# Performance work log

Hardware: AMD Instinct MI355X
Metric: run time of the kernel (lower is better)

The kernel has to match this reference:

```python
import jax, jax.numpy as jnp
import numpy as np

N = 128  # padded Hadamard size (find_min_power(122))
H1 = W1 = 122

def _hadamard(n):
    H = np.array([[1.0]], dtype=np.float32)
    while H.shape[0] < n:
        H = np.block([[H, H], [H, -H]])
    return H

_H = jnp.asarray(_hadamard(N))  # symmetric 128x128 +/-1 matrix
_DN = ('NCHW', 'OIHW', 'NCHW')

def _conv(x, w, b, stride, pad):
    y = jax.lax.conv_general_dilated(x, w, (stride, stride),
                                     [(pad, pad), (pad, pad)], dimension_numbers=_DN)
    return y + b[None, :, None, None]

def _convT(x, w, b, stride, pad):
    # torch ConvTranspose2d weight layout [in, out, kh, kw]
    k = w.shape[-1]
    wf = jnp.flip(w, (2, 3)).transpose(1, 0, 2, 3)  # -> [out, in, kh, kw]
    p = k - 1 - pad
    y = jax.lax.conv_general_dilated(x, wf, (1, 1), [(p, p), (p, p)],
                                     lhs_dilation=(stride, stride), dimension_numbers=_DN)
    return y + b[None, :, None, None]

def _fwht2(x):
    # fwht along -1 then -2 (dense Hadamard matmul, matching fast=False path)
    x = jnp.einsum('bchw,wk->bchk', x, _H)
    return jnp.einsum('bchw,hk->bckw', x, _H)

def _ifwht2(x):
    x = jnp.einsum('bchw,wk->bchk', x, _H) / N
    return jnp.einsum('bchw,hk->bckw', x, _H) / N

def _pad(x):
    return jnp.pad(x, ((0, 0), (0, 0), (0, N - H1), (0, N - W1)))

def _thresh(x, T):
    aT = jnp.abs(T)
    s = jnp.copysign(jax.nn.relu(jnp.abs(x) - aT), x)
    return s + jnp.sign(s) * aT

def _kl(q):
    e = q.size // 64
    p = jax.nn.sigmoid(jnp.full((64,), 0.001, q.dtype))
    qm = jnp.sum(jax.nn.sigmoid(jnp.abs(q).reshape(e, 64)), axis=0) / e
    return jnp.sum(p * jnp.log(p / qm)) + jnp.sum((1 - p) * jnp.log((1 - p) / (1 - qm)))

def _tv(x, weight):
    b, c, h, w = x.shape
    tv = jnp.abs(x[:, :, 1:, :] - x[:, :, :-1, :]).sum() + \
         jnp.abs(x[:, :, :, 1:] - x[:, :, :, :-1]).sum()
    return weight * tv / (b * c * h * w)

def setup_inputs() -> dict:
    key = jax.random.key(0)
    ks = jax.random.split(key, 16)
    B = 128
    inp = {
        'x': jax.random.normal(ks[0], (B, 1, 256, 256), jnp.float32),
        'val': 0,
        'v1': jax.random.uniform(ks[1], (N, N), jnp.float32),
        'T1': jax.random.uniform(ks[2], (N, N), jnp.float32) / 10,
        'v2': jax.random.uniform(ks[3], (N, N), jnp.float32),
        'T2': jax.random.uniform(ks[4], (N, N), jnp.float32) / 10,
        'v3': jax.random.uniform(ks[5], (N, N), jnp.float32),
        'T3': jax.random.uniform(ks[6], (N, N), jnp.float32) / 10,
        'w1': jax.random.normal(ks[7], (4, 1, 16, 16), jnp.float32) * 0.05,
        'b1': jax.random.normal(ks[8], (4,), jnp.float32) * 0.01,
        'w2': jax.random.normal(ks[9], (4, 4, 7, 7), jnp.float32) * 0.05,
        'b2': jax.random.normal(ks[10], (4,), jnp.float32) * 0.01,
        'w3': jax.random.normal(ks[11], (4, 4, 7, 7), jnp.float32) * 0.05,  # [in,out,kh,kw]
        'b3': jax.random.normal(ks[12], (4,), jnp.float32) * 0.01,
        'w4': jax.random.normal(ks[13], (4, 1, 16, 16), jnp.float32) * 0.05,  # [in,out,kh,kw]
        'b4': jax.random.normal(ks[14], (1,), jnp.float32) * 0.01,
    }
    return inp

def reference(x, val, v1, T1, v2, T2, v3, T3, w1, b1, w2, b2, w3, b3, w4, b4):
    TV_WEIGHT = 0.05  # original draws np.random.uniform(0, 0.1); fixed for determinism
    x1 = _conv(x, w1, b1, 2, 1)                       # [B,4,122,122]
    x6 = _thresh(v1 * _fwht2(_pad(x1)), T1)           # [B,4,128,128]
    x9 = _ifwht2(x6)[..., :H1, :W1]
    x10 = _conv(x9, w2, b2, 1, 3)                     # [B,4,122,122]
    x15 = _thresh(v2 * _fwht2(_pad(x10)), T2)
    x18 = _ifwht2(x15)[..., :H1, :W1]
    x19 = _convT(x18, w3, b3, 1, 3) + x10
    x24 = _thresh(v3 * _fwht2(_pad(x19)), T3)
    x27 = _ifwht2(x24 + x6)[..., :H1, :W1]
    out = _convT(x27, w4, b4, 2, 1) * x               # [B,1,256,256]
    loss = 1.0 * _tv(out, TV_WEIGHT) + 0.1 * (_kl(x6) + _kl(x15) + _kl(x24))
    return out, loss
```

## Files before the change

### kernel.cpp

```cpp
#include <hip/hip_runtime.h>
#include <math.h>

#define PLANE 16384
#define NPLANES 512

__device__ __forceinline__ void fwht2d_reg(float* __restrict__ v, float* __restrict__ xch,
                                           int W, int L) {
#pragma unroll
    for (int m = 1; m <= 2; m <<= 1) {
#pragma unroll
        for (int r = 0; r < 64; ++r) {
            if (!(r & m)) {
                int s = r | m;
                float a = v[r], b = v[s];
                v[r] = a + b; v[s] = a - b;
            }
        }
    }
#pragma unroll
    for (int m = 1; m <= 32; m <<= 1) {
        float sg = (L & m) ? -1.f : 1.f;
#pragma unroll
        for (int r = 0; r < 64; ++r) {
            float p = __shfl_xor(v[r], m);
            v[r] = fmaf(sg, v[r], p);
        }
    }
#pragma unroll
    for (int m = 4; m <= 32; m <<= 1) {
#pragma unroll
        for (int r = 0; r < 64; ++r) {
            if (!(r & m)) {
                int s = r | m;
                float a = v[r], b = v[s];
                v[r] = a + b; v[s] = a - b;
            }
        }
    }
    __syncthreads();
#pragma unroll
    for (int j = 0; j < 64; ++j)
        xch[j * 256 + W * 64 + L] = v[j];
    __syncthreads();
    const float s1 = (W & 1) ? -1.f : 1.f;
    const float s2 = (W & 2) ? -1.f : 1.f;
#pragma unroll
    for (int j = 0; j < 64; ++j) {
        const float* row = &xch[j * 256 + L];
        float a0 = row[0], a1 = row[64], a2 = row[128], a3 = row[192];
        float t0 = fmaf(s1, a1, a0);
        float t1 = fmaf(s1, a3, a2);
        v[j] = fmaf(s2, t1, t0);
    }
}

template <bool ADDPOST>
__global__ __launch_bounds__(256) void fwht_kernel_t(
    const float* __restrict__ in, const float* __restrict__ vmat,
    const float* __restrict__ tmat, const float* __restrict__ addbuf,
    float* __restrict__ outInv, float* __restrict__ klpart)
{
    __shared__ float xch[64 * 256];
    const int tid = threadIdx.x;
    const int W = tid >> 6, L = tid & 63;
    const int plane = blockIdx.x;
    const int hbase = W * 32 + ((L >> 5) << 4);
    const int wbase = (L & 31) << 2;
    const float* src = in + (size_t)plane * PLANE;

    float v[64];
#pragma unroll
    for (int g = 0; g < 16; ++g) {
        float4 t = *(const float4*)&src[(hbase + g) * 128 + wbase];
        v[4 * g] = t.x; v[4 * g + 1] = t.y; v[4 * g + 2] = t.z; v[4 * g + 3] = t.w;
    }

    fwht2d_reg(v, xch, W, L);

    float ls0 = 0.f, ls1 = 0.f, ls2 = 0.f, ls3 = 0.f;
#pragma unroll
    for (int g = 0; g < 16; ++g) {
        int rowoff = (hbase + g) * 128 + wbase;
        float4 vm = *(const float4*)&vmat[rowoff];
        float4 tm = *(const float4*)&tmat[rowoff];
        float y0 = v[4 * g]     * vm.x;
        float y1 = v[4 * g + 1] * vm.y;
        float y2 = v[4 * g + 2] * vm.z;
        float y3 = v[4 * g + 3] * vm.w;
        y0 = (fabsf(y0) > fabsf(tm.x)) ? y0 : 0.f;
        y1 = (fabsf(y1) > fabsf(tm.y)) ? y1 : 0.f;
        y2 = (fabsf(y2) > fabsf(tm.z)) ? y2 : 0.f;
        y3 = (fabsf(y3) > fabsf(tm.w)) ? y3 : 0.f;
        ls0 += 1.f / (1.f + __expf(-fabsf(y0)));
        ls1 += 1.f / (1.f + __expf(-fabsf(y1)));
        ls2 += 1.f / (1.f + __expf(-fabsf(y2)));
        ls3 += 1.f / (1.f + __expf(-fabsf(y3)));
        v[4 * g] = y0; v[4 * g + 1] = y1; v[4 * g + 2] = y2; v[4 * g + 3] = y3;
    }
#pragma unroll
    for (int m = 16; m <= 32; m <<= 1) {
        ls0 += __shfl_xor(ls0, m);
        ls1 += __shfl_xor(ls1, m);
        ls2 += __shfl_xor(ls2, m);
        ls3 += __shfl_xor(ls3, m);
    }
    if (L < 16) {
        float4 o; o.x = ls0; o.y = ls1; o.z = ls2; o.w = ls3;
        *(float4*)&klpart[(size_t)(plane * 4 + W) * 64 + 4 * L] = o;
    }

    fwht2d_reg(v, xch, W, L);

    float* dst = outInv + (size_t)plane * PLANE;
    const float s = 1.f / 16384.f;
#pragma unroll
    for (int g = 0; g < 16; ++g) {
        int h = hbase + g;
        int rowoff = h * 128 + wbase;
        bool rv = h < 122;
        float4 ad = make_float4(0.f, 0.f, 0.f, 0.f);
        if (ADDPOST) ad = *(const float4*)&addbuf[(size_t)plane * PLANE + rowoff];
        float4 o;
        o.x = (rv && wbase + 0 < 122) ? fmaf(v[4 * g],     s, ad.x) : 0.f;
        o.y = (rv && wbase + 1 < 122) ? fmaf(v[4 * g + 1], s, ad.y) : 0.f;
        o.z = (rv && wbase + 2 < 122) ? fmaf(v[4 * g + 2], s, ad.z) : 0.f;
        o.w = (rv && wbase + 3 < 122) ? fmaf(v[4 * g + 3], s, ad.w) : 0.f;
        *(float4*)&dst[rowoff] = o;
    }
}

__global__ void prep_weights(const float* __restrict__ w3, const float* __restrict__ w4,
                             float* __restrict__ w3c, float* __restrict__ w4p)
{
    int tid = blockIdx.x * 256 + threadIdx.x;
    if (tid < 784) {
        int oc = tid / 196;
        int rem = tid - oc * 196;
        int ic = rem / 49;
        int k = rem - ic * 49;
        int kh = k / 7, kw = k - kh * 7;
        w3c[(oc * 4 + ic) * 49 + k] = w3[(ic * 4 + oc) * 49 + (6 - kh) * 7 + (6 - kw)];
    }
    if (tid < 1024) {
        int u = tid & 7, t = (tid >> 3) & 7, pb = (tid >> 6) & 1, pa = (tid >> 7) & 1, ic = tid >> 8;
        int kh = 2 * t + (pa ? 0 : 1);
        int kw = 2 * u + (pb ? 0 : 1);
        w4p[tid] = w4[ic * 256 + kh * 16 + kw];
    }
}

__global__ __launch_bounds__(256) void conv1_kernel(
    const float* __restrict__ x, const float* __restrict__ w1,
    const float* __restrict__ b1, float* __restrict__ out)
{
    __shared__ float tile[78][80];
    int tx = blockIdx.x, ty = blockIdx.y, b = blockIdx.z;
    int tid = threadIdx.x;
    const float* xp = x + (size_t)b * 65536;
    int r0g = ty * 64 - 1, c0g = tx * 64 - 1;
    for (int i = tid; i < 78 * 78; i += 256) {
        int rr = i / 78, cc = i - rr * 78;
        int gi = r0g + rr, gj = c0g + cc;
        tile[rr][cc] = (gi >= 0 && gi < 256 && gj >= 0 && gj < 256) ? xp[gi * 256 + gj] : 0.f;
    }
    __syncthreads();
    int cg = tid & 7, r = tid >> 3;
    int B = cg * 4;
    float acc[4][4];
#pragma unroll
    for (int oc = 0; oc < 4; ++oc)
#pragma unroll
        for (int c = 0; c < 4; ++c) acc[oc][c] = 0.f;
#pragma unroll 1
    for (int kh = 0; kh < 16; ++kh) {
        float win[24];
        const float* trow = &tile[2 * r + kh][2 * B];
#pragma unroll
        for (int k = 0; k < 6; ++k)
            *(float4*)&win[4 * k] = *(const float4*)&trow[4 * k];
#pragma unroll
        for (int oc = 0; oc < 4; ++oc) {
            const float* wr = w1 + oc * 256 + kh * 16;
#pragma unroll
            for (int kw = 0; kw < 16; ++kw) {
                float wv = wr[kw];
#pragma unroll
                for (int c = 0; c < 4; ++c)
                    acc[oc][c] = fmaf(win[2 * c + kw], wv, acc[oc][c]);
            }
        }
    }
    int oh = ty * 32 + r;
    int owb = tx * 32 + B;
    bool rowv = oh < 122;
#pragma unroll
    for (int oc = 0; oc < 4; ++oc) {
        float bv = b1[oc];
        float4 res;
        res.x = (rowv && owb + 0 < 122) ? acc[oc][0] + bv : 0.f;
        res.y = (rowv && owb + 1 < 122) ? acc[oc][1] + bv : 0.f;
        res.z = (rowv && owb + 2 < 122) ? acc[oc][2] + bv : 0.f;
        res.w = (rowv && owb + 3 < 122) ? acc[oc][3] + bv : 0.f;
        *(float4*)&out[(((size_t)b * 4 + oc) << 14) + (oh << 7) + owb] = res;
    }
}

__global__ __launch_bounds__(256) void conv7_kernel(
    const float* __restrict__ in, const float* __restrict__ w,
    const float* __restrict__ bias, const float* __restrict__ skip,
    float* __restrict__ out)
{
    __shared__ float tile[4][38][40];
    int tx = blockIdx.x, ty = blockIdx.y, b = blockIdx.z;
    int tid = threadIdx.x;
    int r0g = ty * 32 - 3, c0g = tx * 32 - 3;
    for (int i = tid; i < 4 * 38 * 38; i += 256) {
        int ic = i / 1444;
        int rem = i - ic * 1444;
        int rr = rem / 38, cc = rem - rr * 38;
        int gi = r0g + rr, gj = c0g + cc;
        float v = 0.f;
        if (gi >= 0 && gi < 128 && gj >= 0 && gj < 128)
            v = in[(((size_t)b * 4 + ic) << 14) + (gi << 7) + gj];
        tile[ic][rr][cc] = v;
    }
    __syncthreads();
    int cg = tid & 7, r = tid >> 3;
    int B = cg * 4;
    float acc[4][4];
#pragma unroll
    for (int oc = 0; oc < 4; ++oc)
#pragma unroll
        for (int c = 0; c < 4; ++c) acc[oc][c] = 0.f;
#pragma unroll 1
    for (int ic = 0; ic < 4; ++ic) {
#pragma unroll 1
        for (int kh = 0; kh < 7; ++kh) {
            float win[12];
            const float* trow = &tile[ic][r + kh][B];
#pragma unroll
            for (int k = 0; k < 3; ++k)
                *(float4*)&win[4 * k] = *(const float4*)&trow[4 * k];
#pragma unroll
            for (int oc = 0; oc < 4; ++oc) {
                const float* wr = w + (oc * 4 + ic) * 49 + kh * 7;
#pragma unroll
                for (int kw = 0; kw < 7; ++kw) {
                    float wv = wr[kw];
#pragma unroll
                    for (int c = 0; c < 4; ++c)
                        acc[oc][c] = fmaf(win[c + kw], wv, acc[oc][c]);
                }
            }
        }
    }
    int oh = ty * 32 + r;
    int owb = tx * 32 + B;
    bool rowv = oh < 122;
#pragma unroll
    for (int oc = 0; oc < 4; ++oc) {
        size_t o = (((size_t)b * 4 + oc) << 14) + (oh << 7) + owb;
        float4 sv = make_float4(0.f, 0.f, 0.f, 0.f);
        if (skip) sv = *(const float4*)&skip[o];
        float bv = bias[oc];
        float4 res;
        res.x = (rowv && owb + 0 < 122) ? acc[oc][0] + bv + sv.x : 0.f;
        res.y = (rowv && owb + 1 < 122) ? acc[oc][1] + bv + sv.y : 0.f;
        res.z = (rowv && owb + 2 < 122) ? acc[oc][2] + bv + sv.z : 0.f;
        res.w = (rowv && owb + 3 < 122) ? acc[oc][3] + bv + sv.w : 0.f;
        *(float4*)&out[o] = res;
    }
}

#define CT_HALF(T, ROW, PA)                                                    \
    _Pragma("unroll")                                                          \
    for (int pb = 0; pb < 2; ++pb) {                                           \
        const float* w8 = wp + (((ic * 2 + (PA)) * 2 + pb) * 8 + (T)) * 8;     \
        _Pragma("unroll")                                                      \
        for (int u = 0; u < 8; ++u) {                                          \
            float wv = w8[u];                                                  \
            _Pragma("unroll")                                                  \
            for (int c = 0; c < 4; ++c)                                        \
                acc[PA][pb][c] = fmaf(ROW[8 + c + pb - u], wv, acc[PA][pb][c]);\
        }                                                                      \
    }

__global__ __launch_bounds__(256) void convt4_kernel(
    const float* __restrict__ in, const float* __restrict__ wp,
    const float* __restrict__ bias, const float* __restrict__ xin,
    float* __restrict__ out)
{
    __shared__ float tile[4][40][44];
    int tx = blockIdx.x, ty = blockIdx.y, b = blockIdx.z;
    int tid = threadIdx.x;
    int A0 = ty * 32, B0 = tx * 32;
    int r0g = A0 - 7, c0g = B0 - 8;
    for (int i = tid; i < 4 * 40 * 44; i += 256) {
        int ic = i / 1760;
        int rem = i - ic * 1760;
        int rr = rem / 44, cc = rem - rr * 44;
        int gi = r0g + rr, gj = c0g + cc;
        float v = 0.f;
        if (gi >= 0 && gi < 128 && gj >= 0 && gj < 128)
            v = in[(((size_t)b * 4 + ic) << 14) + (gi << 7) + gj];
        tile[ic][rr][cc] = v;
    }
    __syncthreads();
    int cg = tid & 7, ra = tid >> 3;
    float acc[2][2][4];
#pragma unroll
    for (int pa = 0; pa < 2; ++pa)
#pragma unroll
        for (int pb = 0; pb < 2; ++pb)
#pragma unroll
            for (int c = 0; c < 4; ++c) acc[pa][pb][c] = 0.f;
#pragma unroll 1
    for (int ic = 0; ic < 4; ++ic) {
        float bufA[16], bufB[16];
#pragma unroll
        for (int k = 0; k < 4; ++k)
            *(float4*)&bufB[4 * k] = *(const float4*)&tile[ic][ra + 8][4 * cg + 4 * k];
#pragma unroll 1
        for (int t2 = 0; t2 < 8; t2 += 2) {
#pragma unroll
            for (int k = 0; k < 4; ++k)
                *(float4*)&bufA[4 * k] = *(const float4*)&tile[ic][ra + 7 - t2][4 * cg + 4 * k];
            CT_HALF(t2, bufA, 0)
            CT_HALF(t2, bufB, 1)
#pragma unroll
            for (int k = 0; k < 4; ++k)
                *(float4*)&bufB[4 * k] = *(const float4*)&tile[ic][ra + 6 - t2][4 * cg + 4 * k];
            CT_HALF(t2 + 1, bufB, 0)
            CT_HALF(t2 + 1, bufA, 1)
        }
    }
    int oh0 = 2 * (A0 + ra);
    int owb = 2 * (B0 + 4 * cg);
    float bv = bias[0];
#pragma unroll
    for (int pa = 0; pa < 2; ++pa) {
        size_t o = (size_t)b * 65536 + (size_t)(oh0 + pa) * 256 + owb;
        float4 x0 = *(const float4*)&xin[o];
        float4 x1 = *(const float4*)&xin[o + 4];
        float4 r0, r1;
        r0.x = (acc[pa][0][0] + bv) * x0.x;
        r0.y = (acc[pa][1][0] + bv) * x0.y;
        r0.z = (acc[pa][0][1] + bv) * x0.z;
        r0.w = (acc[pa][1][1] + bv) * x0.w;
        r1.x = (acc[pa][0][2] + bv) * x1.x;
        r1.y = (acc[pa][1][2] + bv) * x1.y;
        r1.z = (acc[pa][0][3] + bv) * x1.z;
        r1.w = (acc[pa][1][3] + bv) * x1.w;
        *(float4*)&out[o] = r0;
        *(float4*)&out[o + 4] = r1;
    }
}

__global__ __launch_bounds__(256) void tv_kernel(
    const float* __restrict__ out, float* __restrict__ tvpart)
{
    const float4* out4 = (const float4*)out;
    __shared__ float red[256];
    int tid = threadIdx.x;
    float local = 0.f;
    const int total4 = 128 * 65536 / 4;
    for (int i4 = blockIdx.x * 256 + tid; i4 < total4; i4 += gridDim.x * 256) {
        float4 a = out4[i4];
        int i = i4 << 2;
        local += fabsf(a.y - a.x) + fabsf(a.z - a.y) + fabsf(a.w - a.z);
        if ((i & 255) != 252) local += fabsf(out[i + 4] - a.w);
        if ((i & 65535) < 65280) {
            float4 c = out4[i4 + 64];
            local += fabsf(c.x - a.x) + fabsf(c.y - a.y) + fabsf(c.z - a.z) + fabsf(c.w - a.w);
        }
    }
    red[tid] = local;
    __syncthreads();
    for (int s = 128; s > 0; s >>= 1) {
        if (tid < s) red[tid] += red[tid + s];
        __syncthreads();
    }
    if (tid == 0) tvpart[blockIdx.x] = red[0];
}

__global__ __launch_bounds__(256) void reduce1_kernel(
    const float* __restrict__ klpart, const float* __restrict__ tvpart,
    float* __restrict__ klred, float* __restrict__ tvred)
{
    int bid = blockIdx.x;
    int tid = threadIdx.x;
    if (bid < 48) {
        int layer = bid >> 4, chunk = bid & 15;
        int sub = tid >> 6, t = tid & 63;
        const float* base = klpart + (size_t)layer * 131072 + (size_t)chunk * 128 * 64;
        float s = 0.f;
        for (int r = sub; r < 128; r += 4)
            s += base[r * 64 + t];
        __shared__ float red[4][64];
        red[sub][t] = s;
        __syncthreads();
        if (tid < 64)
            klred[(layer * 16 + chunk) * 64 + tid] =
                red[0][tid] + red[1][tid] + red[2][tid] + red[3][tid];
    } else {
        __shared__ float red[256];
        float s = 0.f;
        for (int i = tid; i < 2048; i += 256) s += tvpart[i];
        red[tid] = s;
        __syncthreads();
        for (int st = 128; st > 0; st >>= 1) {
            if (tid < st) red[tid] += red[tid + st];
            __syncthreads();
        }
        if (tid == 0) tvred[0] = red[0];
    }
}

__global__ __launch_bounds__(64) void finalize2_kernel(
    const float* __restrict__ klred, const float* __restrict__ tvred,
    float* __restrict__ lossout)
{
    int t = threadIdx.x;
    float p = 1.f / (1.f + __expf(-0.001f));
    float term = 0.f;
#pragma unroll
    for (int l = 0; l < 3; ++l) {
        float q = 0.f;
#pragma unroll
        for (int c = 0; c < 16; ++c)
            q += klred[(l * 16 + c) * 64 + t];
        float qm = q * (1.f / 131072.f);
        term += p * logf(p / qm) + (1.f - p) * logf((1.f - p) / (1.f - qm));
    }
#pragma unroll
    for (int off = 32; off > 0; off >>= 1)
        term += __shfl_down(term, off);
    if (t == 0)
        lossout[0] = 0.05f * tvred[0] / 8388608.f + 0.1f * term;
}

extern "C" void kernel_launch(void* const* d_in, const int* in_sizes, int n_in,
                              void* d_out, int out_size, void* d_ws, size_t ws_size,
                              hipStream_t stream) {
    (void)in_sizes; (void)n_in; (void)out_size; (void)ws_size;
    const float* x  = (const float*)d_in[0];
    const float* v1 = (const float*)d_in[2];
    const float* T1 = (const float*)d_in[3];
    const float* v2 = (const float*)d_in[4];
    const float* T2 = (const float*)d_in[5];
    const float* v3 = (const float*)d_in[6];
    const float* T3 = (const float*)d_in[7];
    const float* w1 = (const float*)d_in[8];
    const float* b1 = (const float*)d_in[9];
    const float* w2 = (const float*)d_in[10];
    const float* b2 = (const float*)d_in[11];
    const float* w3 = (const float*)d_in[12];
    const float* b3 = (const float*)d_in[13];
    const float* w4 = (const float*)d_in[14];
    const float* b4 = (const float*)d_in[15];
    float* out = (float*)d_out;

    float* W0 = (float*)d_ws;
    float* W1 = W0 + (size_t)NPLANES * PLANE;
    float* W2 = W1 + (size_t)NPLANES * PLANE;
    float* klpart = W2 + (size_t)NPLANES * PLANE;
    float* tvpart = klpart + 3 * 2048 * 64;
    float* klred  = tvpart + 2048;
    float* tvred  = klred + 3072;
    float* w3c = tvred + 64;
    float* w4p = w3c + 784;
    float* x10buf = out;

    prep_weights<<<4, 256, 0, stream>>>(w3, w4, w3c, w4p);
    conv1_kernel<<<dim3(4, 4, 128), 256, 0, stream>>>(x, w1, b1, W0);
    fwht_kernel_t<false><<<NPLANES, 256, 0, stream>>>(W0, v1, T1, nullptr, W1, klpart);
    conv7_kernel<<<dim3(4, 4, 128), 256, 0, stream>>>(W1, w2, b2, nullptr, x10buf);
    fwht_kernel_t<false><<<NPLANES, 256, 0, stream>>>(x10buf, v2, T2, nullptr, W0, klpart + 131072);
    conv7_kernel<<<dim3(4, 4, 128), 256, 0, stream>>>(W0, w3c, b3, x10buf, W2);
    fwht_kernel_t<true><<<NPLANES, 256, 0, stream>>>(W2, v3, T3, W1, W0, klpart + 2 * 131072);
    convt4_kernel<<<dim3(4, 4, 128), 256, 0, stream>>>(W0, w4p, b4, x, out);
    tv_kernel<<<2048, 256, 0, stream>>>(out, tvpart);
    reduce1_kernel<<<49, 256, 0, stream>>>(klpart, tvpart, klred, tvred);
    finalize2_kernel<<<1, 64, 0, stream>>>(klred, tvred, out + 8388608);
}
```

Measured before the change: 441.3 us.

## Restructure 2D FWHT as row/column passes with LDS transpose

Rewrites the FWHT kernel so each pair of threads owns one 128-wide row: a 64-point register Hadamard plus one xor-1 shuffle finishes each 1D transform, and a padded LDS transpose switches between row and column passes. This replaces the earlier scheme of 32 cross-lane shuffle rounds plus a 64 KB LDS exchange with 4-way combines. The per-plane KL partial layout shrinks to half as many rows, and the reduction kernel and workspace offsets are adjusted to match. In the column pass the v/T loads become strided scalar loads, and LDS column accesses with pitch 132 may cause bank conflicts.

```diff
diff --git a/kernel.cpp b/kernel.cpp
--- a/kernel.cpp
+++ b/kernel.cpp
@@ -4,10 +4,9 @@
 #define PLANE 16384
 #define NPLANES 512
 
-__device__ __forceinline__ void fwht2d_reg(float* __restrict__ v, float* __restrict__ xch,
-                                           int W, int L) {
-#pragma unroll
-    for (int m = 1; m <= 2; m <<= 1) {
+__device__ __forceinline__ void had64(float* __restrict__ v) {
+#pragma unroll
+    for (int m = 1; m <= 32; m <<= 1) {
 #pragma unroll
         for (int r = 0; r < 64; ++r) {
             if (!(r & m)) {
@@ -17,42 +16,17 @@
             }
         }
     }
-#pragma unroll
-    for (int m = 1; m <= 32; m <<= 1) {
-        float sg = (L & m) ? -1.f : 1.f;
-#pragma unroll
-        for (int r = 0; r < 64; ++r) {
-            float p = __shfl_xor(v[r], m);
-            v[r] = fmaf(sg, v[r], p);
-        }
-    }
-#pragma unroll
-    for (int m = 4; m <= 32; m <<= 1) {
-#pragma unroll
-        for (int r = 0; r < 64; ++r) {
-            if (!(r & m)) {
-                int s = r | m;
-                float a = v[r], b = v[s];
-                v[r] = a + b; v[s] = a - b;
-            }
-        }
-    }
-    __syncthreads();
-#pragma unroll
-    for (int j = 0; j < 64; ++j)
-        xch[j * 256 + W * 64 + L] = v[j];
-    __syncthreads();
-    const float s1 = (W & 1) ? -1.f : 1.f;
-    const float s2 = (W & 2) ? -1.f : 1.f;
+}
+
+__device__ __forceinline__ void bit6x(float* __restrict__ v, float sg) {
 #pragma unroll
     for (int j = 0; j < 64; ++j) {
-        const float* row = &xch[j * 256 + L];
-        float a0 = row[0], a1 = row[64], a2 = row[128], a3 = row[192];
-        float t0 = fmaf(s1, a1, a0);
-        float t1 = fmaf(s1, a3, a2);
-        v[j] = fmaf(s2, t1, t0);
-    }
-}
+        float p = __shfl_xor(v[j], 1);
+        v[j] = fmaf(sg, v[j], p);
+    }
+}
+
+#define LPITCH 132
 
 template <bool ADDPOST>
 __global__ __launch_bounds__(256) void fwht_kernel_t(
@@ -60,71 +34,75 @@
     const float* __restrict__ tmat, const float* __restrict__ addbuf,
     float* __restrict__ outInv, float* __restrict__ klpart)
 {
-    __shared__ float xch[64 * 256];
-    const int tid = threadIdx.x;
-    const int W = tid >> 6, L = tid & 63;
+    __shared__ float lds[128 * LPITCH];
+    const int t = threadIdx.x;
+    const int r = t >> 1;
+    const int hf = t & 1;
+    const float sg = hf ? -1.f : 1.f;
     const int plane = blockIdx.x;
-    const int hbase = W * 32 + ((L >> 5) << 4);
-    const int wbase = (L & 31) << 2;
     const float* src = in + (size_t)plane * PLANE;
 
     float v[64];
 #pragma unroll
-    for (int g = 0; g < 16; ++g) {
-        float4 t = *(const float4*)&src[(hbase + g) * 128 + wbase];
-        v[4 * g] = t.x; v[4 * g + 1] = t.y; v[4 * g + 2] = t.z; v[4 * g + 3] = t.w;
-    }
-
-    fwht2d_reg(v, xch, W, L);
-
-    float ls0 = 0.f, ls1 = 0.f, ls2 = 0.f, ls3 = 0.f;
-#pragma unroll
-    for (int g = 0; g < 16; ++g) {
-        int rowoff = (hbase + g) * 128 + wbase;
-        float4 vm = *(const float4*)&vmat[rowoff];
-        float4 tm = *(const float4*)&tmat[rowoff];
-        float y0 = v[4 * g]     * vm.x;
-        float y1 = v[4 * g + 1] * vm.y;
-        float y2 = v[4 * g + 2] * vm.z;
-        float y3 = v[4 * g + 3] * vm.w;
-        y0 = (fabsf(y0) > fabsf(tm.x)) ? y0 : 0.f;
-        y1 = (fabsf(y1) > fabsf(tm.y)) ? y1 : 0.f;
-        y2 = (fabsf(y2) > fabsf(tm.z)) ? y2 : 0.f;
-        y3 = (fabsf(y3) > fabsf(tm.w)) ? y3 : 0.f;
-        ls0 += 1.f / (1.f + __expf(-fabsf(y0)));
-        ls1 += 1.f / (1.f + __expf(-fabsf(y1)));
-        ls2 += 1.f / (1.f + __expf(-fabsf(y2)));
-        ls3 += 1.f / (1.f + __expf(-fabsf(y3)));
-        v[4 * g] = y0; v[4 * g + 1] = y1; v[4 * g + 2] = y2; v[4 * g + 3] = y3;
-    }
-#pragma unroll
-    for (int m = 16; m <= 32; m <<= 1) {
-        ls0 += __shfl_xor(ls0, m);
-        ls1 += __shfl_xor(ls1, m);
-        ls2 += __shfl_xor(ls2, m);
-        ls3 += __shfl_xor(ls3, m);
-    }
-    if (L < 16) {
-        float4 o; o.x = ls0; o.y = ls1; o.z = ls2; o.w = ls3;
-        *(float4*)&klpart[(size_t)(plane * 4 + W) * 64 + 4 * L] = o;
-    }
-
-    fwht2d_reg(v, xch, W, L);
+    for (int k = 0; k < 16; ++k)
+        *(float4*)&v[4 * k] = *(const float4*)&src[r * 128 + hf * 64 + 4 * k];
+
+    had64(v); bit6x(v, sg);
+
+#pragma unroll
+    for (int k = 0; k < 16; ++k)
+        *(float4*)&lds[r * LPITCH + hf * 64 + 4 * k] = *(const float4*)&v[4 * k];
+    __syncthreads();
+#pragma unroll
+    for (int j = 0; j < 64; ++j)
+        v[j] = lds[(hf * 64 + j) * LPITCH + r];
+
+    had64(v); bit6x(v, sg);
+
+    float ls = 0.f;
+#pragma unroll
+    for (int j = 0; j < 64; ++j) {
+        int idx = (hf * 64 + j) * 128 + r;
+        float y = v[j] * vmat[idx];
+        float tt = fabsf(tmat[idx]);
+        y = (fabsf(y) > tt) ? y : 0.f;
+        ls += 1.f / (1.f + __expf(-fabsf(y)));
+        v[j] = y;
+    }
+    ls += __shfl_xor(ls, 1);
+    {
+        int W = t >> 6;
+        if (hf == 0)
+            klpart[(size_t)(plane * 2 + (W >> 1)) * 64 + (r & 63)] = ls;
+    }
+
+    had64(v); bit6x(v, sg);
+
+    __syncthreads();
+#pragma unroll
+    for (int j = 0; j < 64; ++j)
+        lds[(hf * 64 + j) * LPITCH + r] = v[j];
+    __syncthreads();
+#pragma unroll
+    for (int k = 0; k < 16; ++k)
+        *(float4*)&v[4 * k] = *(const float4*)&lds[r * LPITCH + hf * 64 + 4 * k];
+
+    had64(v); bit6x(v, sg);
 
     float* dst = outInv + (size_t)plane * PLANE;
     const float s = 1.f / 16384.f;
-#pragma unroll
-    for (int g = 0; g < 16; ++g) {
-        int h = hbase + g;
-        int rowoff = h * 128 + wbase;
-        bool rv = h < 122;
+    bool rowv = r < 122;
+#pragma unroll
+    for (int k = 0; k < 16; ++k) {
+        int wb = hf * 64 + 4 * k;
+        int rowoff = r * 128 + wb;
         float4 ad = make_float4(0.f, 0.f, 0.f, 0.f);
         if (ADDPOST) ad = *(const float4*)&addbuf[(size_t)plane * PLANE + rowoff];
         float4 o;
-        o.x = (rv && wbase + 0 < 122) ? fmaf(v[4 * g],     s, ad.x) : 0.f;
-        o.y = (rv && wbase + 1 < 122) ? fmaf(v[4 * g + 1], s, ad.y) : 0.f;
-        o.z = (rv && wbase + 2 < 122) ? fmaf(v[4 * g + 2], s, ad.z) : 0.f;
-        o.w = (rv && wbase + 3 < 122) ? fmaf(v[4 * g + 3], s, ad.w) : 0.f;
+        o.x = (rowv && wb + 0 < 122) ? fmaf(v[4 * k],     s, ad.x) : 0.f;
+        o.y = (rowv && wb + 1 < 122) ? fmaf(v[4 * k + 1], s, ad.y) : 0.f;
+        o.z = (rowv && wb + 2 < 122) ? fmaf(v[4 * k + 2], s, ad.z) : 0.f;
+        o.w = (rowv && wb + 3 < 122) ? fmaf(v[4 * k + 3], s, ad.w) : 0.f;
         *(float4*)&dst[rowoff] = o;
     }
 }
@@ -392,9 +370,9 @@
     if (bid < 48) {
         int layer = bid >> 4, chunk = bid & 15;
         int sub = tid >> 6, t = tid & 63;
-        const float* base = klpart + (size_t)layer * 131072 + (size_t)chunk * 128 * 64;
+        const float* base = klpart + (size_t)layer * 65536 + (size_t)chunk * 64 * 64;
         float s = 0.f;
-        for (int r = sub; r < 128; r += 4)
+        for (int r = sub; r < 64; r += 4)
             s += base[r * 64 + t];
         __shared__ float red[4][64];
         red[sub][t] = s;
@@ -464,7 +442,7 @@
     float* W1 = W0 + (size_t)NPLANES * PLANE;
     float* W2 = W1 + (size_t)NPLANES * PLANE;
     float* klpart = W2 + (size_t)NPLANES * PLANE;
-    float* tvpart = klpart + 3 * 2048 * 64;
+    float* tvpart = klpart + 3 * 1024 * 64;
     float* klred  = tvpart + 2048;
     float* tvred  = klred + 3072;
     float* w3c = tvred + 64;
@@ -475,9 +453,9 @@
     conv1_kernel<<<dim3(4, 4, 128), 256, 0, stream>>>(x, w1, b1, W0);
     fwht_kernel_t<false><<<NPLANES, 256, 0, stream>>>(W0, v1, T1, nullptr, W1, klpart);
     conv7_kernel<<<dim3(4, 4, 128), 256, 0, stream>>>(W1, w2, b2, nullptr, x10buf);
-    fwht_kernel_t<false><<<NPLANES, 256, 0, stream>>>(x10buf, v2, T2, nullptr, W0, klpart + 131072);
+    fwht_kernel_t<false><<<NPLANES, 256, 0, stream>>>(x10buf, v2, T2, nullptr, W0, klpart + 65536);
     conv7_kernel<<<dim3(4, 4, 128), 256, 0, stream>>>(W0, w3c, b3, x10buf, W2);
-    fwht_kernel_t<true><<<NPLANES, 256, 0, stream>>>(W2, v3, T3, W1, W0, klpart + 2 * 131072);
+    fwht_kernel_t<true><<<NPLANES, 256, 0, stream>>>(W2, v3, T3, W1, W0, klpart + 2 * 65536);
     convt4_kernel<<<dim3(4, 4, 128), 256, 0, stream>>>(W0, w4p, b4, x, out);
     tv_kernel<<<2048, 256, 0, stream>>>(out, tvpart);
     reduce1_kernel<<<49, 256, 0, stream>>>(klpart, tvpart, klred, tvred);
```

Result: faster. 412.6 us (-6.5%).
